# Performance work log

Measured on AMD Instinct MI355X. Metric: run time of the kernel, lower is better.

Reference implementation:

```python
import jax, jax.numpy as jnp
import numpy as np

B, T, IN, H, LAYERS = 32, 512, 512, 512, 2


def _lstm_dir(x, Wx, Wh, b, reverse):
    """AugmentedLstm with highway, one direction.
    x: (B,T,I), Wx: (I,6H), Wh: (H,5H), b: (5H). Returns (B,T,H), h_final, c_final."""
    h = Wh.shape[0]
    # precompute input projections for all timesteps: (T,B,6H)
    px = jnp.einsum('bti,ig->tbg', x, Wx)
    if reverse:
        px = px[::-1]
    bsz = x.shape[0]
    h0 = jnp.zeros((bsz, h), x.dtype)
    c0 = jnp.zeros((bsz, h), x.dtype)

    def step(carry, pxt):
        hp, cp = carry
        ps = hp @ Wh + b  # (B,5H)
        i = jax.nn.sigmoid(pxt[:, 0*h:1*h] + ps[:, 0*h:1*h])
        f = jax.nn.sigmoid(pxt[:, 1*h:2*h] + ps[:, 1*h:2*h])
        g = jnp.tanh(pxt[:, 2*h:3*h] + ps[:, 2*h:3*h])
        o = jax.nn.sigmoid(pxt[:, 3*h:4*h] + ps[:, 3*h:4*h])
        c = i * g + f * cp
        ht = o * jnp.tanh(c)
        # highway: gate*h_t + (1-gate)*(W_x2 x_t)
        r = jax.nn.sigmoid(pxt[:, 4*h:5*h] + ps[:, 4*h:5*h])
        ht = r * ht + (1.0 - r) * pxt[:, 5*h:6*h]
        return (ht, c), ht

    (hf, cf), ys = jax.lax.scan(step, (h0, c0), px)
    if reverse:
        ys = ys[::-1]
    return jnp.transpose(ys, (1, 0, 2)), hf, cf


def setup_inputs() -> dict:
    key = jax.random.key(0)
    ks = jax.random.split(key, 16)
    d = {'x': jax.random.normal(ks[0], (B, T, IN), jnp.float32)}
    in_sizes = [IN, 2 * H]
    i = 1
    for l in range(LAYERS):
        isz = in_sizes[l]
        for dname in ('f', 'b'):
            d[f'Wx{l}{dname}'] = jax.random.normal(ks[i], (isz, 6 * H), jnp.float32) / np.sqrt(isz); i += 1
            d[f'Wh{l}{dname}'] = jax.random.normal(ks[i], (H, 5 * H), jnp.float32) / np.sqrt(H); i += 1
            d[f'b{l}{dname}'] = jnp.zeros((5 * H,), jnp.float32)
    return d


def reference(x, Wx0f, Wh0f, b0f, Wx0b, Wh0b, b0b,
              Wx1f, Wh1f, b1f, Wx1b, Wh1b, b1b):
    params = [((Wx0f, Wh0f, b0f), (Wx0b, Wh0b, b0b)),
              ((Wx1f, Wh1f, b1f), (Wx1b, Wh1b, b1b))]
    out = x
    final_h, final_c = [], []
    for (pf, pb) in params:
        yf, hf, cf = _lstm_dir(out, *pf, reverse=False)
        yb, hb, cb = _lstm_dir(out, *pb, reverse=True)
        out = jnp.concatenate([yf, yb], axis=-1)  # (B,T,2H)
        final_h.append(jnp.concatenate([hf, hb], axis=-1)[None])  # (1,B,2H)
        final_c.append(jnp.concatenate([cf, cb], axis=-1)[None])
    # torch code cats per-layer (1,B,2H) states along dim=1 -> (1, layers*B, 2H)
    final_h = jnp.concatenate(final_h, axis=1)
    final_c = jnp.concatenate(final_c, axis=1)
    return out, final_h, final_c
```

## Files before the change

### kernel.cpp

```cpp
#include <hip/hip_runtime.h>


typedef float f32x4 __attribute__((ext_vector_type(4)));
typedef __bf16 bf16x8 __attribute__((ext_vector_type(8)));
typedef unsigned short us8 __attribute__((ext_vector_type(8)));
typedef unsigned short us4 __attribute__((ext_vector_type(4)));
typedef unsigned int u32x4 __attribute__((ext_vector_type(4)));

__device__ __forceinline__ unsigned short f2bf(float f) {
  unsigned int u = __float_as_uint(f);
  u += 0x7FFFu + ((u >> 16) & 1u);
  return (unsigned short)(u >> 16);
}
__device__ __forceinline__ float bf2f(unsigned int h) {
  return __uint_as_float(h << 16);
}
__device__ __forceinline__ float sigf(float x) { return 1.0f / (1.0f + __expf(-x)); }
__device__ __forceinline__ float tanh_(float x) { return 2.0f / (1.0f + __expf(-2.0f * x)) - 1.0f; }

#define MFMA(a, b, c) __builtin_amdgcn_mfma_f32_16x16x32_bf16((a), (b), (c), 0, 0, 0)
#define GLOAD_LDS(gp, lp)                                                           \
  __builtin_amdgcn_global_load_lds(                                                 \
      (const __attribute__((address_space(1))) void*)(gp),                          \
      (__attribute__((address_space(3))) void*)(lp), 16, 0, 0)

__device__ __forceinline__ void chunk1_ld(const char* p, u32x4& v) {
  asm volatile("global_load_dwordx4 %0, %1, off sc0 sc1"
               : "=&v"(v) : "v"(p) : "memory");
}
__device__ __forceinline__ void pub16(char* p, u32x4 v) {
  asm volatile("global_store_dwordx4 %0, %1, off sc0 sc1" :: "v"(p), "v"(v) : "memory");
}


__global__ void k_convert_x(const float* __restrict__ x, unsigned short* __restrict__ xb, int n4) {
  int i = blockIdx.x * blockDim.x + threadIdx.x;
  if (i < n4) {
    float4 v = ((const float4*)x)[i];
    us4 o;
    o[0] = f2bf(v.x); o[1] = f2bf(v.y); o[2] = f2bf(v.z); o[3] = f2bf(v.w);
    ((us4*)xb)[i] = o;
  }
}

__global__ __launch_bounds__(256) void k_pack_wxT(
    const float* __restrict__ W0, const float* __restrict__ W1,
    const float* __restrict__ W2, const float* __restrict__ W3,
    unsigned short* __restrict__ o01, unsigned short* __restrict__ o23) {
  int y = blockIdx.z;
  int K = (y >> 1) ? 1024 : 512;
  int kb = blockIdx.y * 32;
  if (kb >= K) return;
  const float* W = (y == 0) ? W0 : (y == 1) ? W1 : (y == 2) ? W2 : W3;
  unsigned short* o = (y >> 1) ? (o23 + (size_t)(y & 1) * 3072 * 1024)
                               : (o01 + (size_t)(y & 1) * 3072 * 512);
  __shared__ float tile[32][33];
  int nb = blockIdx.x * 32;
  int tx = threadIdx.x & 31, ty = threadIdx.x >> 5;
#pragma unroll
  for (int r = 0; r < 4; ++r)
    tile[ty + r * 8][tx] = W[(size_t)(kb + ty + r * 8) * 3072 + nb + tx];
  __syncthreads();
#pragma unroll
  for (int r = 0; r < 4; ++r)
    o[(size_t)(nb + ty + r * 8) * K + kb + tx] = f2bf(tile[tx][ty + r * 8]);
}

__global__ void k_pack_whp(const float* __restrict__ W0, const float* __restrict__ W1,
                           const float* __restrict__ W2, const float* __restrict__ W3,
                           unsigned short* __restrict__ out) {
  int y = blockIdx.y;
  const float* W = (y == 0) ? W0 : (y == 1) ? W1 : (y == 2) ? W2 : W3;
  unsigned short* o = out + (size_t)y * 1310720;
  int v = blockIdx.x * 256 + threadIdx.x;
  int lane = v & 63, ks = (v >> 6) & 15, ns = (v >> 10) & 31, g = v >> 15;
  int col = g * 512 + ns * 16 + (lane & 15);
  int kb = ks * 32 + ((lane >> 4) << 3);
  us8 vec;
#pragma unroll
  for (int e = 0; e < 8; ++e) vec[e] = f2bf(W[(size_t)(kb + e) * 2560 + col]);
  *(us8*)&o[(size_t)v * 8] = vec;
}

__global__ __launch_bounds__(256) void k_gemm(const unsigned short* __restrict__ A,
                                              const unsigned short* __restrict__ BtBase,
                                              unsigned short* __restrict__ CBase, int K) {
  __shared__ __align__(128) unsigned short As[128 * 32];
  __shared__ __align__(128) unsigned short Bs[128 * 32];
  const unsigned short* Bt = BtBase + (size_t)blockIdx.z * 3072 * K;
  unsigned short* C = CBase + (size_t)blockIdx.z * 16384 * 3072;
  int tid = threadIdx.x;
  int w = tid >> 6, l = tid & 63;
  int m0 = blockIdx.x * 128, n0 = blockIdx.y * 128;
  int wr = (w >> 1) * 64, wc = (w & 1) * 64;
  f32x4 acc[4][4];
#pragma unroll
  for (int i = 0; i < 4; ++i)
#pragma unroll
    for (int j = 0; j < 4; ++j) acc[i][j] = (f32x4){0.f, 0.f, 0.f, 0.f};

  for (int k0 = 0; k0 < K; k0 += 32) {
    __syncthreads();
#pragma unroll
    for (int half = 0; half < 2; ++half) {
      int r = w * 32 + half * 16 + (l >> 2);
      int gq = (l & 3) ^ (r & 3);
      GLOAD_LDS(A + (size_t)(m0 + r) * K + k0 + gq * 8, &As[(w * 32 + half * 16) * 32]);
      GLOAD_LDS(Bt + (size_t)(n0 + r) * K + k0 + gq * 8, &Bs[(w * 32 + half * 16) * 32]);
    }
    __syncthreads();
    bf16x8 af[4], bfr[4];
#pragma unroll
    for (int mi = 0; mi < 4; ++mi) {
      int r = wr + mi * 16 + (l & 15);
      int q = (l >> 4) ^ (r & 3);
      af[mi] = __builtin_bit_cast(bf16x8, *(const us8*)&As[r * 32 + q * 8]);
    }
#pragma unroll
    for (int ni = 0; ni < 4; ++ni) {
      int r = wc + ni * 16 + (l & 15);
      int q = (l >> 4) ^ (r & 3);
      bfr[ni] = __builtin_bit_cast(bf16x8, *(const us8*)&Bs[r * 32 + q * 8]);
    }
#pragma unroll
    for (int mi = 0; mi < 4; ++mi)
#pragma unroll
      for (int ni = 0; ni < 4; ++ni) acc[mi][ni] = MFMA(af[mi], bfr[ni], acc[mi][ni]);
  }
#pragma unroll
  for (int mi = 0; mi < 4; ++mi)
#pragma unroll
    for (int ni = 0; ni < 4; ++ni)
#pragma unroll
      for (int r4 = 0; r4 < 4; ++r4) {
        int row = m0 + wr + mi * 16 + (l >> 4) * 4 + r4;
        int rr = ((row & 511) << 5) + (row >> 9);
        int col = n0 + wc + ni * 16 + (l & 15);
        C[(size_t)rr * 3072 + col] = f2bf(acc[mi][ni][r4]);
      }
}

__global__ __launch_bounds__(512, 1) void k_persist(
    const unsigned short* __restrict__ px,
    const unsigned short* __restrict__ wp,
    const float* __restrict__ bias_f, const float* __restrict__ bias_b,
    char* __restrict__ hxc,
    unsigned short* __restrict__ ybf,
    float* __restrict__ yf,
    float* __restrict__ finals,
    int layer) {
  __shared__ float part[2][4][8][160];
  __shared__ unsigned short hl[8 * 520];
  int wg = blockIdx.x;
  int grp = wg >> 4, m = wg & 15;
  int d = grp & 1, q = grp >> 1;
  int tid = threadIdx.x;
  int w = tid >> 6, l = tid & 63;
  int kh = w & 3, nh = w >> 2;
  int ns = m * 2 + nh;
  const unsigned short* wpd = wp + (size_t)d * 1310720;
  const unsigned short* pxd = px + (size_t)d * 16384 * 3072;
  const float* bias = d ? bias_b : bias_f;
  char* hxg = hxc + (size_t)layer * 196608 + (size_t)grp * 12288;

  bf16x8 wf[5][4];
#pragma unroll
  for (int g5 = 0; g5 < 5; ++g5)
#pragma unroll
    for (int kk = 0; kk < 4; ++kk)
      wf[g5][kk] = __builtin_bit_cast(
          bf16x8,
          *(const us8*)&wpd[(size_t)((g5 * 32 + ns) * 16 + (kh * 4 + kk)) * 512 + l * 8]);

  bool epi = tid < 256;
  int r = tid >> 5, j = tid & 31, jg = m * 32 + j, b = q * 8 + r;
  float bv[5];
#pragma unroll
  for (int g5 = 0; g5 < 5; ++g5) bv[g5] = bias[(g5 << 9) + jg];

  float c = 0.f;
  unsigned int xCur[6], xNext[6];
  if (epi) {
    int t0 = d ? 511 : 0;
    const unsigned short* pp = pxd + ((size_t)((t0 << 5) + b)) * 3072 + jg;
#pragma unroll
    for (int q6 = 0; q6 < 6; ++q6) xNext[q6] = pp[q6 << 9];
  }

  int c0 = tid;
  int c1 = 512 + tid;
  bool has1 = tid < 256;
  int m8r0 = c0 / 6, myc0 = c0 - m8r0 * 6;
  int off0 = (m8r0 & 7) * 520 + (m8r0 >> 3) * 32 + myc0 * 6;
  bool is5_0 = (myc0 == 5);
  int m8r1 = c1 / 6, myc1 = c1 - m8r1 * 6;
  int off1 = (m8r1 & 7) * 520 + (m8r1 >> 3) * 32 + myc1 * 6;
  bool is5_1 = (myc1 == 5);

  int fbase = (l & 7) * 520 + kh * 128 + ((l >> 4) << 3);

  int myc = l & 31, pbase = l & 32, prow = 2 * w + (l >> 5);

  for (int s = 0; s < 512; ++s) {
    int t = d ? (511 - s) : s;

    if (s > 0) {
      const char* cb = hxg + (size_t)(s & 1) * 98304;
      const char* a0 = cb + (size_t)c0 * 16;
      const char* a1 = cb + (size_t)c1 * 16;
      unsigned enc = (unsigned)(s | ((~s & 0xFFFF) << 16));
      u32x4 v0, v1;
      bool d0 = false, d1 = !has1;
      long guard = 0;
      bool first = true, ok;
      do {
        if (!first) __builtin_amdgcn_s_sleep(1);
        first = false;
        if (!d0) chunk1_ld(a0, v0);
        if (!d1) chunk1_ld(a1, v1);
        asm volatile("s_waitcnt vmcnt(0)" ::: "memory");
        __builtin_amdgcn_sched_barrier(0);
        d0 = d0 || (v0[3] == enc);
        d1 = d1 || (v1[3] == enc);
        ok = (__all((int)(d0 && d1)) != 0);
      } while (!ok && ++guard < 300000L);
      {
        unsigned int* pw = (unsigned int*)((char*)hl + off0 * 2);
        pw[0] = v0[0];
        if (!is5_0) { pw[1] = v0[1]; pw[2] = v0[2]; }
        if (has1) {
          unsigned int* pw1 = (unsigned int*)((char*)hl + off1 * 2);
          pw1[0] = v1[0];
          if (!is5_1) { pw1[1] = v1[1]; pw1[2] = v1[2]; }
        }
      }
    }

    if (epi) {
#pragma unroll
      for (int i = 0; i < 6; ++i) xCur[i] = xNext[i];
      if (s < 511) {
        int tn = d ? (511 - (s + 1)) : (s + 1);
        const unsigned short* pp = pxd + ((size_t)((tn << 5) + b)) * 3072 + jg;
#pragma unroll
        for (int q6 = 0; q6 < 6; ++q6) xNext[q6] = pp[q6 << 9];
      }
    }

    __syncthreads();

    f32x4 acc[5];
#pragma unroll
    for (int g5 = 0; g5 < 5; ++g5) acc[g5] = (f32x4){0.f, 0.f, 0.f, 0.f};
    if (s > 0) {
#pragma unroll
      for (int kk = 0; kk < 4; ++kk) {
        bf16x8 av = __builtin_bit_cast(bf16x8, *(const us8*)&hl[fbase + kk * 32]);
#pragma unroll
        for (int g5 = 0; g5 < 5; ++g5) acc[g5] = MFMA(av, wf[g5][kk], acc[g5]);
      }
    }
    if (l < 32) {
#pragma unroll
      for (int g5 = 0; g5 < 5; ++g5)
#pragma unroll
        for (int r4 = 0; r4 < 4; ++r4)
          part[s & 1][kh][(l >> 4) * 4 + r4][nh * 80 + g5 * 16 + (l & 15)] = acc[g5][r4];
    }
    __syncthreads();

    if (epi) {
      int cc0 = (j >> 4) * 80 + (j & 15);
      float ps_[5];
#pragma unroll
      for (int g5 = 0; g5 < 5; ++g5) {
        int cc = cc0 + g5 * 16;
        ps_[g5] = part[s & 1][0][r][cc] + part[s & 1][1][r][cc] +
                  part[s & 1][2][r][cc] + part[s & 1][3][r][cc] + bv[g5];
      }
      float x0 = bf2f(xCur[0]), x1 = bf2f(xCur[1]), x2 = bf2f(xCur[2]);
      float x3 = bf2f(xCur[3]), x4 = bf2f(xCur[4]), x5 = bf2f(xCur[5]);
      float iG = sigf(x0 + ps_[0]);
      float fG = sigf(x1 + ps_[1]);
      float gG = tanh_(x2 + ps_[2]);
      float oG = sigf(x3 + ps_[3]);
      float cn = iG * gG + fG * c;
      c = cn;
      float ht = oG * tanh_(cn);
      float rG = sigf(x4 + ps_[4]);
      ht = rG * ht + (1.f - rG) * x5;

      if (s < 511) {
        unsigned int hbits = (unsigned int)f2bf(ht);
        unsigned int vv[6];
#pragma unroll
        for (int i = 0; i < 6; ++i)
          vv[i] = __shfl(hbits, (pbase + myc * 6 + i) & 63);
        unsigned int pw0 = vv[0] | (vv[1] << 16);
        unsigned int pw1 = vv[2] | (vv[3] << 16);
        unsigned int pw2 = vv[4] | (vv[5] << 16);
        if (myc == 5) { pw1 = 0; pw2 = 0; }
        if (myc < 6) {
          char* dst = hxg + (size_t)((s + 1) & 1) * 98304 +
                      (size_t)((m * 8 + prow) * 6 + myc) * 16;
          unsigned enc1 = (unsigned)((s + 1) | ((~(s + 1) & 0xFFFF) << 16));
          u32x4 pv = {pw0, pw1, pw2, enc1};
          pub16(dst, pv);
        }
      }

      size_t yo = ((size_t)(b * 512 + t)) * 1024 + d * 512 + jg;
      if (ybf) ybf[yo] = f2bf(ht);
      else     yf[yo] = ht;
      if (s == 511) {
        int fo = (layer * 32 + b) * 1024 + d * 512 + jg;
        finals[fo] = ht;
        finals[65536 + fo] = cn;
      }
    }
  }
}


extern "C" void kernel_launch(void* const* d_in, const int* in_sizes, int n_in,
                              void* d_out, int out_size, void* d_ws, size_t ws_size,
                              hipStream_t stream) {
  (void)in_sizes; (void)n_in; (void)out_size; (void)ws_size;
  const float* x = (const float*)d_in[0];
  const float* Wx[4] = {(const float*)d_in[1], (const float*)d_in[4],
                        (const float*)d_in[7], (const float*)d_in[10]};
  const float* Wh[4] = {(const float*)d_in[2], (const float*)d_in[5],
                        (const float*)d_in[8], (const float*)d_in[11]};
  const float* bs[4] = {(const float*)d_in[3], (const float*)d_in[6],
                        (const float*)d_in[9], (const float*)d_in[12]};

  char* ws = (char*)d_ws;
  unsigned short* px   = (unsigned short*)(ws);
  unsigned short* whp  = (unsigned short*)(ws + 201326592);
  char*           hxc  = (char*)(ws + 211812352);

  char* ob = (char*)d_out;
  unsigned short* xbf  = (unsigned short*)(ob);
  unsigned short* wxt0 = (unsigned short*)(ob + 16777216);
  unsigned short* wxt1 = (unsigned short*)(ob + 33554432);
  unsigned short* a1bf = (unsigned short*)(ob);
  float* out = (float*)d_out;
  float* finals = out + 16777216;

  k_convert_x<<<8192, 256, 0, stream>>>(x, xbf, 2097152);
  k_pack_wxT<<<dim3(96, 32, 4), 256, 0, stream>>>(Wx[0], Wx[1], Wx[2], Wx[3], wxt0, wxt1);
  k_pack_whp<<<dim3(640, 4), 256, 0, stream>>>(Wh[0], Wh[1], Wh[2], Wh[3], whp);
  hipMemsetAsync(hxc, 0xFF, 393216, stream);

  for (int layer = 0; layer < 2; ++layer) {
    int K = layer ? 1024 : 512;
    const unsigned short* Ag = layer ? a1bf : xbf;
    const unsigned short* wxt = layer ? wxt1 : wxt0;
    k_gemm<<<dim3(128, 24, 2), 256, 0, stream>>>(Ag, wxt, px, K);
    k_persist<<<128, 512, 0, stream>>>(
        px, whp + (size_t)layer * 2621440, bs[layer * 2], bs[layer * 2 + 1],
        hxc, layer ? nullptr : a1bf, layer ? out : nullptr, finals, layer);
  }
}
```

Measured before the change: 2.704 ms.

## Halve persistent LSTM grid and drop cross-wave K-split reduction

The persistent recurrent kernel now runs 64 workgroups of 256 threads instead of 128 of 512. Each wave holds the full K=512 slice of its Wh columns in registers (80 bf16x8 fragments), which removes the LDS partial-sum buffer and the second barrier per step. Each lane computes the gates for two batch rows, the h exchange uses 4 chunks per thread with a double-buffered LDS tile, and step tags continue across layers so the flag buffer no longer needs per-layer regions. This trades fewer barriers and fewer inter-block sync participants for much higher register pressure and more MFMA and epilogue work per wave.

```diff
diff --git a/kernel.cpp b/kernel.cpp
--- a/kernel.cpp
+++ b/kernel.cpp
@@ -140,7 +140,7 @@
       }
 }
 
-__global__ __launch_bounds__(512, 1) void k_persist(
+__global__ __launch_bounds__(256, 1) void k_persist(
     const unsigned short* __restrict__ px,
     const unsigned short* __restrict__ wp,
     const float* __restrict__ bias_f, const float* __restrict__ bias_b,
@@ -149,102 +149,110 @@
     float* __restrict__ yf,
     float* __restrict__ finals,
     int layer) {
-  __shared__ float part[2][4][8][160];
-  __shared__ unsigned short hl[8 * 520];
+  __shared__ unsigned short hl[2][8 * 520];
   int wg = blockIdx.x;
-  int grp = wg >> 4, m = wg & 15;
+  int grp = wg >> 3, m = wg & 7;
   int d = grp & 1, q = grp >> 1;
   int tid = threadIdx.x;
-  int w = tid >> 6, l = tid & 63;
-  int kh = w & 3, nh = w >> 2;
-  int ns = m * 2 + nh;
+  int wv = tid >> 6, l = tid & 63;
+  int ns = m * 4 + wv;
   const unsigned short* wpd = wp + (size_t)d * 1310720;
   const unsigned short* pxd = px + (size_t)d * 16384 * 3072;
   const float* bias = d ? bias_b : bias_f;
-  char* hxg = hxc + (size_t)layer * 196608 + (size_t)grp * 12288;
-
-  bf16x8 wf[5][4];
+  char* hxg = hxc + (size_t)grp * 16384;
+
+  bf16x8 wf[5][16];
 #pragma unroll
   for (int g5 = 0; g5 < 5; ++g5)
 #pragma unroll
-    for (int kk = 0; kk < 4; ++kk)
-      wf[g5][kk] = __builtin_bit_cast(
-          bf16x8,
-          *(const us8*)&wpd[(size_t)((g5 * 32 + ns) * 16 + (kh * 4 + kk)) * 512 + l * 8]);
-
-  bool epi = tid < 256;
-  int r = tid >> 5, j = tid & 31, jg = m * 32 + j, b = q * 8 + r;
+    for (int kf = 0; kf < 16; ++kf)
+      wf[g5][kf] = __builtin_bit_cast(
+          bf16x8, *(const us8*)&wpd[(size_t)((g5 * 32 + ns) * 16 + kf) * 512 + l * 8]);
+
+  int hsel = l >> 4;
+  int r0 = (hsel == 0) ? 0 : (hsel == 1) ? 4 : (hsel == 2) ? 2 : 6;
+  int r1 = r0 + 1;
+  bool hi2 = (hsel & 2) != 0;
+  int j = l & 15, jg = m * 64 + wv * 16 + j;
+  int b0 = q * 8 + r0, b1 = q * 8 + r1;
   float bv[5];
 #pragma unroll
   for (int g5 = 0; g5 < 5; ++g5) bv[g5] = bias[(g5 << 9) + jg];
 
-  float c = 0.f;
-  unsigned int xCur[6], xNext[6];
-  if (epi) {
+  float c0 = 0.f, c1 = 0.f;
+  unsigned int xC0[6], xN0[6], xC1[6], xN1[6];
+  {
     int t0 = d ? 511 : 0;
-    const unsigned short* pp = pxd + ((size_t)((t0 << 5) + b)) * 3072 + jg;
-#pragma unroll
-    for (int q6 = 0; q6 < 6; ++q6) xNext[q6] = pp[q6 << 9];
-  }
-
-  int c0 = tid;
-  int c1 = 512 + tid;
-  bool has1 = tid < 256;
-  int m8r0 = c0 / 6, myc0 = c0 - m8r0 * 6;
-  int off0 = (m8r0 & 7) * 520 + (m8r0 >> 3) * 32 + myc0 * 6;
-  bool is5_0 = (myc0 == 5);
-  int m8r1 = c1 / 6, myc1 = c1 - m8r1 * 6;
-  int off1 = (m8r1 & 7) * 520 + (m8r1 >> 3) * 32 + myc1 * 6;
-  bool is5_1 = (myc1 == 5);
-
-  int fbase = (l & 7) * 520 + kh * 128 + ((l >> 4) << 3);
-
-  int myc = l & 31, pbase = l & 32, prow = 2 * w + (l >> 5);
+    const unsigned short* p0 = pxd + ((size_t)((t0 << 5) + b0)) * 3072 + jg;
+    const unsigned short* p1 = pxd + ((size_t)((t0 << 5) + b1)) * 3072 + jg;
+#pragma unroll
+    for (int q6 = 0; q6 < 6; ++q6) { xN0[q6] = p0[q6 << 9]; xN1[q6] = p1[q6 << 9]; }
+  }
+
+  int cs0 = tid, cs1 = tid + 256, cs2 = tid + 512, cs3 = tid + 768;
+  int dep0 = ((cs0 >> 4) & 7) * 520 + (cs0 >> 7) * 64 + (cs0 & 15) * 4;
+  int dep1 = ((cs1 >> 4) & 7) * 520 + (cs1 >> 7) * 64 + (cs1 & 15) * 4;
+  int dep2 = ((cs2 >> 4) & 7) * 520 + (cs2 >> 7) * 64 + (cs2 & 15) * 4;
+  int dep3 = ((cs3 >> 4) & 7) * 520 + (cs3 >> 7) * 64 + (cs3 & 15) * 4;
+
+  int pr = l >> 2, pcq = l & 3;
+  int pbaseL = ((pr & 2) ? 32 : 0) + ((pr & 4) ? 16 : 0);
+  bool prOdd = (pr & 1) != 0;
+
+  int abase = (l & 7) * 520 + ((l >> 4) << 3);
+
+  int Sbase = layer * 512;
 
   for (int s = 0; s < 512; ++s) {
     int t = d ? (511 - s) : s;
+    int par = s & 1;
 
     if (s > 0) {
-      const char* cb = hxg + (size_t)(s & 1) * 98304;
-      const char* a0 = cb + (size_t)c0 * 16;
-      const char* a1 = cb + (size_t)c1 * 16;
-      unsigned enc = (unsigned)(s | ((~s & 0xFFFF) << 16));
-      u32x4 v0, v1;
-      bool d0 = false, d1 = !has1;
+      const char* cb = hxg + (size_t)par * 131072;
+      unsigned S = (unsigned)(Sbase + s);
+      unsigned enc = S | ((~S & 0xFFFF) << 16);
+      u32x4 v0, v1, v2, v3;
       long guard = 0;
       bool first = true, ok;
       do {
         if (!first) __builtin_amdgcn_s_sleep(1);
         first = false;
-        if (!d0) chunk1_ld(a0, v0);
-        if (!d1) chunk1_ld(a1, v1);
+        chunk1_ld(cb + (size_t)cs0 * 16, v0);
+        chunk1_ld(cb + (size_t)cs1 * 16, v1);
+        chunk1_ld(cb + (size_t)cs2 * 16, v2);
+        chunk1_ld(cb + (size_t)cs3 * 16, v3);
         asm volatile("s_waitcnt vmcnt(0)" ::: "memory");
         __builtin_amdgcn_sched_barrier(0);
-        d0 = d0 || (v0[3] == enc);
-        d1 = d1 || (v1[3] == enc);
-        ok = (__all((int)(d0 && d1)) != 0);
+        bool mine = (v0[3] == enc) && (v1[3] == enc) &&
+                    (v2[3] == enc) && (v3[3] == enc);
+        ok = (__all((int)mine) != 0);
       } while (!ok && ++guard < 300000L);
       {
-        unsigned int* pw = (unsigned int*)((char*)hl + off0 * 2);
-        pw[0] = v0[0];
-        if (!is5_0) { pw[1] = v0[1]; pw[2] = v0[2]; }
-        if (has1) {
-          unsigned int* pw1 = (unsigned int*)((char*)hl + off1 * 2);
-          pw1[0] = v1[0];
-          if (!is5_1) { pw1[1] = v1[1]; pw1[2] = v1[2]; }
-        }
-      }
-    }
-
-    if (epi) {
-#pragma unroll
-      for (int i = 0; i < 6; ++i) xCur[i] = xNext[i];
-      if (s < 511) {
-        int tn = d ? (511 - (s + 1)) : (s + 1);
-        const unsigned short* pp = pxd + ((size_t)((tn << 5) + b)) * 3072 + jg;
-#pragma unroll
-        for (int q6 = 0; q6 < 6; ++q6) xNext[q6] = pp[q6 << 9];
-      }
+        unsigned int* pw = (unsigned int*)&hl[par][dep0];
+        pw[0] = v0[0]; pw[1] = v0[1];
+      }
+      {
+        unsigned int* pw = (unsigned int*)&hl[par][dep1];
+        pw[0] = v1[0]; pw[1] = v1[1];
+      }
+      {
+        unsigned int* pw = (unsigned int*)&hl[par][dep2];
+        pw[0] = v2[0]; pw[1] = v2[1];
+      }
+      {
+        unsigned int* pw = (unsigned int*)&hl[par][dep3];
+        pw[0] = v3[0]; pw[1] = v3[1];
+      }
+    }
+
+#pragma unroll
+    for (int i = 0; i < 6; ++i) { xC0[i] = xN0[i]; xC1[i] = xN1[i]; }
+    if (s < 511) {
+      int tn = d ? (511 - (s + 1)) : (s + 1);
+      const unsigned short* p0 = pxd + ((size_t)((tn << 5) + b0)) * 3072 + jg;
+      const unsigned short* p1 = pxd + ((size_t)((tn << 5) + b1)) * 3072 + jg;
+#pragma unroll
+      for (int q6 = 0; q6 < 6; ++q6) { xN0[q6] = p0[q6 << 9]; xN1[q6] = p1[q6 << 9]; }
     }
 
     __syncthreads();
@@ -254,69 +262,77 @@
     for (int g5 = 0; g5 < 5; ++g5) acc[g5] = (f32x4){0.f, 0.f, 0.f, 0.f};
     if (s > 0) {
 #pragma unroll
-      for (int kk = 0; kk < 4; ++kk) {
-        bf16x8 av = __builtin_bit_cast(bf16x8, *(const us8*)&hl[fbase + kk * 32]);
-#pragma unroll
-        for (int g5 = 0; g5 < 5; ++g5) acc[g5] = MFMA(av, wf[g5][kk], acc[g5]);
-      }
-    }
-    if (l < 32) {
-#pragma unroll
-      for (int g5 = 0; g5 < 5; ++g5)
-#pragma unroll
-        for (int r4 = 0; r4 < 4; ++r4)
-          part[s & 1][kh][(l >> 4) * 4 + r4][nh * 80 + g5 * 16 + (l & 15)] = acc[g5][r4];
-    }
-    __syncthreads();
-
-    if (epi) {
-      int cc0 = (j >> 4) * 80 + (j & 15);
-      float ps_[5];
-#pragma unroll
-      for (int g5 = 0; g5 < 5; ++g5) {
-        int cc = cc0 + g5 * 16;
-        ps_[g5] = part[s & 1][0][r][cc] + part[s & 1][1][r][cc] +
-                  part[s & 1][2][r][cc] + part[s & 1][3][r][cc] + bv[g5];
-      }
-      float x0 = bf2f(xCur[0]), x1 = bf2f(xCur[1]), x2 = bf2f(xCur[2]);
-      float x3 = bf2f(xCur[3]), x4 = bf2f(xCur[4]), x5 = bf2f(xCur[5]);
-      float iG = sigf(x0 + ps_[0]);
-      float fG = sigf(x1 + ps_[1]);
-      float gG = tanh_(x2 + ps_[2]);
-      float oG = sigf(x3 + ps_[3]);
-      float cn = iG * gG + fG * c;
-      c = cn;
-      float ht = oG * tanh_(cn);
-      float rG = sigf(x4 + ps_[4]);
-      ht = rG * ht + (1.f - rG) * x5;
-
-      if (s < 511) {
-        unsigned int hbits = (unsigned int)f2bf(ht);
-        unsigned int vv[6];
-#pragma unroll
-        for (int i = 0; i < 6; ++i)
-          vv[i] = __shfl(hbits, (pbase + myc * 6 + i) & 63);
-        unsigned int pw0 = vv[0] | (vv[1] << 16);
-        unsigned int pw1 = vv[2] | (vv[3] << 16);
-        unsigned int pw2 = vv[4] | (vv[5] << 16);
-        if (myc == 5) { pw1 = 0; pw2 = 0; }
-        if (myc < 6) {
-          char* dst = hxg + (size_t)((s + 1) & 1) * 98304 +
-                      (size_t)((m * 8 + prow) * 6 + myc) * 16;
-          unsigned enc1 = (unsigned)((s + 1) | ((~(s + 1) & 0xFFFF) << 16));
-          u32x4 pv = {pw0, pw1, pw2, enc1};
-          pub16(dst, pv);
-        }
-      }
-
-      size_t yo = ((size_t)(b * 512 + t)) * 1024 + d * 512 + jg;
-      if (ybf) ybf[yo] = f2bf(ht);
-      else     yf[yo] = ht;
-      if (s == 511) {
-        int fo = (layer * 32 + b) * 1024 + d * 512 + jg;
-        finals[fo] = ht;
-        finals[65536 + fo] = cn;
-      }
+      for (int kf = 0; kf < 16; ++kf) {
+        bf16x8 av = __builtin_bit_cast(bf16x8, *(const us8*)&hl[par][abase + kf * 32]);
+#pragma unroll
+        for (int g5 = 0; g5 < 5; ++g5) acc[g5] = MFMA(av, wf[g5][kf], acc[g5]);
+      }
+    }
+
+    float ps0[5], ps1[5];
+#pragma unroll
+    for (int g5 = 0; g5 < 5; ++g5) {
+      ps0[g5] = (hi2 ? acc[g5][2] : acc[g5][0]) + bv[g5];
+      ps1[g5] = (hi2 ? acc[g5][3] : acc[g5][1]) + bv[g5];
+    }
+    float ht0, ht1, cn0, cn1;
+    {
+      float x0 = bf2f(xC0[0]), x1 = bf2f(xC0[1]), x2 = bf2f(xC0[2]);
+      float x3 = bf2f(xC0[3]), x4 = bf2f(xC0[4]), x5 = bf2f(xC0[5]);
+      float iG = sigf(x0 + ps0[0]);
+      float fG = sigf(x1 + ps0[1]);
+      float gG = tanh_(x2 + ps0[2]);
+      float oG = sigf(x3 + ps0[3]);
+      cn0 = iG * gG + fG * c0;
+      c0 = cn0;
+      ht0 = oG * tanh_(cn0);
+      float rG = sigf(x4 + ps0[4]);
+      ht0 = rG * ht0 + (1.f - rG) * x5;
+    }
+    {
+      float x0 = bf2f(xC1[0]), x1 = bf2f(xC1[1]), x2 = bf2f(xC1[2]);
+      float x3 = bf2f(xC1[3]), x4 = bf2f(xC1[4]), x5 = bf2f(xC1[5]);
+      float iG = sigf(x0 + ps1[0]);
+      float fG = sigf(x1 + ps1[1]);
+      float gG = tanh_(x2 + ps1[2]);
+      float oG = sigf(x3 + ps1[3]);
+      cn1 = iG * gG + fG * c1;
+      c1 = cn1;
+      ht1 = oG * tanh_(cn1);
+      float rG = sigf(x4 + ps1[4]);
+      ht1 = rG * ht1 + (1.f - rG) * x5;
+    }
+
+    unsigned int h0b = (unsigned int)f2bf(ht0);
+    unsigned int h1b = (unsigned int)f2bf(ht1);
+    if (s < 511) {
+      unsigned int vals[4];
+#pragma unroll
+      for (int e4 = 0; e4 < 4; ++e4) {
+        int srcl = pbaseL + pcq * 4 + e4;
+        unsigned int a = __shfl(h0b, srcl);
+        unsigned int bq = __shfl(h1b, srcl);
+        vals[e4] = prOdd ? bq : a;
+      }
+      if (l < 32) {
+        unsigned S1 = (unsigned)(Sbase + s + 1);
+        unsigned enc1 = S1 | ((~S1 & 0xFFFF) << 16);
+        char* dst = hxg + (size_t)((s + 1) & 1) * 131072 +
+                    (size_t)(((m * 8 + pr) * 16) + wv * 4 + pcq) * 16;
+        u32x4 pv = {vals[0] | (vals[1] << 16), vals[2] | (vals[3] << 16), 0u, enc1};
+        pub16(dst, pv);
+      }
+    }
+
+    size_t yo0 = ((size_t)(b0 * 512 + t)) * 1024 + d * 512 + jg;
+    size_t yo1 = ((size_t)(b1 * 512 + t)) * 1024 + d * 512 + jg;
+    if (ybf) { ybf[yo0] = (unsigned short)h0b; ybf[yo1] = (unsigned short)h1b; }
+    else     { yf[yo0] = ht0; yf[yo1] = ht1; }
+    if (s == 511) {
+      int fo0 = (layer * 32 + b0) * 1024 + d * 512 + jg;
+      int fo1 = (layer * 32 + b1) * 1024 + d * 512 + jg;
+      finals[fo0] = ht0; finals[65536 + fo0] = cn0;
+      finals[fo1] = ht1; finals[65536 + fo1] = cn1;
     }
   }
 }
@@ -350,14 +366,14 @@
   k_convert_x<<<8192, 256, 0, stream>>>(x, xbf, 2097152);
   k_pack_wxT<<<dim3(96, 32, 4), 256, 0, stream>>>(Wx[0], Wx[1], Wx[2], Wx[3], wxt0, wxt1);
   k_pack_whp<<<dim3(640, 4), 256, 0, stream>>>(Wh[0], Wh[1], Wh[2], Wh[3], whp);
-  hipMemsetAsync(hxc, 0xFF, 393216, stream);
+  hipMemsetAsync(hxc, 0xFF, 262144, stream);
 
   for (int layer = 0; layer < 2; ++layer) {
     int K = layer ? 1024 : 512;
     const unsigned short* Ag = layer ? a1bf : xbf;
     const unsigned short* wxt = layer ? wxt1 : wxt0;
     k_gemm<<<dim3(128, 24, 2), 256, 0, stream>>>(Ag, wxt, px, K);
-    k_persist<<<128, 512, 0, stream>>>(
+    k_persist<<<64, 256, 0, stream>>>(
         px, whp + (size_t)layer * 2621440, bs[layer * 2], bs[layer * 2 + 1],
         hxc, layer ? nullptr : a1bf, layer ? out : nullptr, finals, layer);
   }
```

Result: slower. 4.615 ms (+70.7%).
